# Optimization experiments

Hardware: AMD Instinct MI355X
Metric: run time of the kernel (lower is better)

Reference implementation:

```python
import jax, jax.numpy as jnp
import numpy as np

K = 3          # B-spline order (cubic)
G = 10         # number of spline intervals over [0, 1]
NELY, NELX = 512, 512
WIDTHS = [2, 32, 32, 1]


def _make_grid(in_dim):
    # extended uniform knot vector over [0,1] with K extra knots each side: (in_dim, G+2K+1)
    h = 1.0 / G
    knots = jnp.arange(-K, G + K + 1, dtype=jnp.float32) * h
    return jnp.tile(knots[None, :], (in_dim, 1))


def setup_inputs() -> dict:
    key = jax.random.key(0)
    ks = jax.random.split(key, 1 + 3 * (len(WIDTHS) - 1))
    inp = {"coords": jax.random.uniform(ks[0], (NELY * NELX, 2), dtype=jnp.float32)}
    for l, (i, o) in enumerate(zip(WIDTHS[:-1], WIDTHS[1:])):
        inp[f"grid{l}"] = _make_grid(i)
        inp[f"coef{l}"] = 0.1 * jax.random.normal(ks[1 + 3 * l], (i, o, G + K), dtype=jnp.float32)
        inp[f"sb{l}"] = jax.random.normal(ks[2 + 3 * l], (i, o), dtype=jnp.float32) / np.sqrt(i).astype(np.float32)
        inp[f"sp{l}"] = jnp.ones((i, o), dtype=jnp.float32)
    inp["density_bias"] = jnp.full((1,), np.float32(np.log(0.5 / (1.0 - 0.5 + 1e-8))))
    return inp


def _b_batch(x, grid):
    # Cox-de Boor recursion. x: (B, in), grid: (in, G+2K+1) -> bases (B, in, G+K)
    xe = x[:, :, None]
    v = ((xe >= grid[None, :, :-1]) & (xe < grid[None, :, 1:])).astype(x.dtype)
    for p in range(1, K + 1):
        left = (xe - grid[None, :, : -(p + 1)]) / (grid[None, :, p:-1] - grid[None, :, : -(p + 1)])
        right = (grid[None, :, p + 1:] - xe) / (grid[None, :, p + 1:] - grid[None, :, 1:-p])
        v = left * v[:, :, :-1] + right * v[:, :, 1:]
    return v


def _kan_layer(x, grid, coef, sb, sp):
    # y_out = sum_in [ sb * silu(x) + sp * sum_k B_k(x) * coef_k ]
    B = _b_batch(x, grid)                               # (batch, in, G+K)
    spline = jnp.einsum('bik,iok->bio', B, coef)        # (batch, in, out)
    base = jax.nn.silu(x)                               # (batch, in)
    return jnp.sum(sb[None] * base[:, :, None] + sp[None] * spline, axis=1)


def reference(coords, grid0, coef0, sb0, sp0, grid1, coef1, sb1, sp1,
              grid2, coef2, sb2, sp2, density_bias):
    h = _kan_layer(coords, grid0, coef0, sb0, sp0)
    h = _kan_layer(h, grid1, coef1, sb1, sp1)
    logits = _kan_layer(h, grid2, coef2, sb2, sp2) + density_bias
    return jax.nn.sigmoid(logits).reshape(1, NELY, NELX)
```

## Files before the change

kernel.cpp:

```cpp
#include <hip/hip_runtime.h>
#include <hip/hip_bf16.h>

typedef __hip_bfloat16 bf16;
typedef __fp16 h2v __attribute__((ext_vector_type(2)));
typedef __fp16 half8 __attribute__((ext_vector_type(8)));
typedef float floatx4 __attribute__((ext_vector_type(4)));

#define NPTS (512*512)

#define OFF_BIAS 12
#define OFF_FLAG 13
#define OFF_BF   16
#define NFRAG    50
#define WS_WORDS (16 + NFRAG*64*4)


__device__ __forceinline__ bool sniff_f32(const void* g0) {
    float f = ((const float*)g0)[0];
    return fabsf(f + 0.3f) < 0.01f;
}
__device__ __forceinline__ float ld(const void* p, int i, bool f32) {
    return f32 ? ((const float*)p)[i] : __bfloat162float(((const bf16*)p)[i]);
}
__device__ __forceinline__ unsigned pk_rtn(float a, float b) {
    union { h2v v; unsigned u; } x;
    x.v[0] = (__fp16)a; x.v[1] = (__fp16)b;
    return x.u;
}
__device__ __forceinline__ unsigned pkf16(float a, float b) {
    union { h2v v; unsigned u; } x;
    x.v = __builtin_amdgcn_cvt_pkrtz(a, b);
    return x.u;
}

__device__ float slotval(int layer, int K, int o,
                         const void* c0, const void* sb0, const void* sp0,
                         const void* c1, const void* sb1, const void* sp1,
                         const void* c2, const void* sb2, const void* sp2, bool f32)
{
    int i = K >> 4, s = K & 15;
    if (layer == 2 && o != 0) return 0.0f;
    if (s >= 1 && s <= 13) {
        int m = s - 1;
        if (layer == 0) return ld(c0, (i*32+o)*13 + m, f32) * ld(sp0, i*32+o, f32);
        if (layer == 1) return ld(c1, (i*32+o)*13 + m, f32) * ld(sp1, i*32+o, f32);
        return ld(c2, i*13 + m, f32) * ld(sp2, i, f32);
    }
    if (s == 14) {
        if (layer == 0) return ld(sb0, i*32+o, f32);
        if (layer == 1) return ld(sb1, i*32+o, f32);
        return ld(sb2, i, f32);
    }
    return 0.0f;
}

__global__ __launch_bounds__(256) void kan_prep(
    const void* __restrict__ g0, const void* __restrict__ c0,
    const void* __restrict__ sb0, const void* __restrict__ sp0,
    const void* __restrict__ g1, const void* __restrict__ c1,
    const void* __restrict__ sb1, const void* __restrict__ sp1,
    const void* __restrict__ g2, const void* __restrict__ c2,
    const void* __restrict__ sb2, const void* __restrict__ sp2,
    const void* __restrict__ bias, float* __restrict__ ws)
{
    const bool f32 = sniff_f32(g0);
    int t = blockIdx.x * blockDim.x + threadIdx.x;

    if (t < 16) {
        if (t < 12) {
            int l = t >> 2, j = t & 3;
            const void* g = (l == 0) ? g0 : (l == 1) ? g1 : g2;
            float lo = ld(g, 0, f32), hi = ld(g, 16, f32);
            float ih = 16.0f / (hi - lo);
            float v = (j == 0) ? lo : (j == 1) ? hi
                    : (j == 2) ? ih : (-lo * ih);
            ws[t] = v;
        } else if (t == 12) ws[12] = ld(bias, 0, f32);
        else if (t == 13)   ws[13] = f32 ? 1.0f : 0.0f;
        else                ws[t] = 0.0f;
        return;
    }
    int ft = t - 16;
    if (ft >= NFRAG * 64) return;
    int f = ft >> 6, l = ft & 63, n = l & 15, q = l >> 4;
    int layer, c, nt;
    if (f < 2)       { layer = 0; c = 0;          nt = f; }
    else if (f < 34) { layer = 1; c = (f - 2) >> 1; nt = (f - 2) & 1; }
    else             { layer = 2; c = f - 34;     nt = 0; }
    int o = nt * 16 + n;
    unsigned wv[4];
#pragma unroll
    for (int jp = 0; jp < 4; jp++) {
        int K0 = c * 32 + q * 8 + jp * 2;
        float v0 = slotval(layer, K0,     o, c0,sb0,sp0, c1,sb1,sp1, c2,sb2,sp2, f32);
        float v1 = slotval(layer, K0 + 1, o, c0,sb0,sp0, c1,sb1,sp1, c2,sb2,sp2, f32);
        wv[jp] = pk_rtn(v0, v1);
    }
    uint4 out4; out4.x = wv[0]; out4.y = wv[1]; out4.z = wv[2]; out4.w = wv[3];
    ((uint4*)((unsigned*)ws + OFF_BF))[f * 64 + l] = out4;
}

__device__ __forceinline__ floatx4 mf(uint4 a, uint4 b, floatx4 c)
{
    union { uint4 u; half8 h; } ua, ub;
    ua.u = a; ub.u = b;
    return __builtin_amdgcn_mfma_f32_16x16x32_f16(ua.h, ub.h, c, 0, 0, 0);
}

__device__ __forceinline__ void eval_taps(float x, float ngh, float ih,
    unsigned& A, unsigned& B, unsigned& C, int& wout, float& si)
{
    float t  = fmaf(x, ih, ngh);
    float fj = floorf(t);
    float u  = t - fj;
    bool inb = (t >= 0.0f) && (t < 16.0f);
    float s6 = inb ? 0.166666667f : 0.0f;
    int jc = min(max((int)fj, 0), 15);
    float u2 = u * u, u3 = u2 * u, om = 1.0f - u;
    float b0 = om * om * om * s6;
    float b1 = (fmaf(3.0f, u3, 4.0f) - 6.0f * u2) * s6;
    float b2 = fmaf(-3.0f, u3, fmaf(3.0f, u2, fmaf(3.0f, u, 1.0f))) * s6;
    float b3 = u3 * s6;
    int s0 = jc - 2;
    wout = ((s0 + 2) >> 1) - 1;
    if (s0 & 1) { A = pkf16(0.0f, b0); B = pkf16(b1, b2); C = pkf16(b3, 0.0f); }
    else        { A = pkf16(b0, b1);   B = pkf16(b2, b3); C = 0u; }
    si = x / (1.0f + __expf(-x));
}

struct TapPack {
    unsigned A0, B0, C0, A1, B1, C1, S0, S1;
    int w0, w1;
};

__device__ __forceinline__ TapPack eval2(float f0, float f1,
                                         float ngh, float ih)
{
    TapPack t;
    float si0, si1;
    eval_taps(f0, ngh, ih, t.A0, t.B0, t.C0, t.w0, si0);
    eval_taps(f1, ngh, ih, t.A1, t.B1, t.C1, t.w1, si1);
    t.S0 = pkf16(si0, 0.0f);
    t.S1 = pkf16(si1, 0.0f);
    return t;
}

__device__ __forceinline__ void commit(unsigned* row, const TapPack& t)
{
    uint4 z; z.x = 0u; z.y = 0u; z.z = 0u; z.w = 0u;
    *(uint4*)(row + 0)  = z;
    *(uint4*)(row + 4)  = z;
    *(uint4*)(row + 8)  = z;
    *(uint4*)(row + 12) = z;
    row[t.w0 < 0 ? 18 : t.w0] = t.A0;
    row[t.w0 + 1]  = t.B0;
    row[t.w0 + 2]  = t.C0;
    row[8 + t.w1]  = t.A1;
    row[9 + t.w1]  = t.B1;
    row[10 + t.w1] = t.C1;
    row[7]  = t.S0;
    row[15] = t.S1;
}

__global__ __launch_bounds__(256, 4) void kan_main(
    const void* __restrict__ coords, const float* __restrict__ ws,
    void* __restrict__ out)
{
    __shared__ __align__(16) unsigned lds[4 * 1280];
    const unsigned* wsu = (const unsigned*)ws;
    const uint4* bfp = (const uint4*)(wsu + OFF_BF);

    int tid = threadIdx.x;
    int l = tid & 63, w = tid >> 6;
    int p = blockIdx.x * 256 + w * 64 + l;

    unsigned* rb = lds + w * 1280;
    unsigned* cb = rb;
    unsigned* myrow = cb + l * 20;

    const bool f32 = (ws[OFF_FLAG] != 0.0f);
    float x0, x1;
    if (f32) {
        float2 c = ((const float2*)coords)[p];
        x0 = c.x; x1 = c.y;
    } else {
        unsigned cc = ((const unsigned*)coords)[p];
        union { unsigned u; float f; } cv;
        cv.u = (cc & 0xffffu) << 16;  x0 = cv.f;
        cv.u = cc & 0xffff0000u;      x1 = cv.f;
    }

    const float iha = ws[2],  ngha = ws[3];
    const float ihb = ws[6],  nghb = ws[7];
    const float ihc = ws[10], nghc = ws[11];

    const int arow = l & 15, aq = (l >> 4) * 4;
    const int drow = (l >> 4) * 4, dcol = l & 15;

    float h[32];

    {
        floatx4 acc[4][2];
#pragma unroll
        for (int mt = 0; mt < 4; mt++)
#pragma unroll
            for (int nt = 0; nt < 2; nt++) acc[mt][nt] = (floatx4)0.0f;

        uint4 bf0 = bfp[0 * 64 + l], bf1 = bfp[1 * 64 + l];
        TapPack t0 = eval2(x0, x1, ngha, iha);
        commit(myrow, t0);
#pragma unroll
        for (int mt = 0; mt < 4; mt++) {
            uint4 a = *(const uint4*)(cb + (arow + 16 * mt) * 20 + aq);
            acc[mt][0] = mf(a, bf0, acc[mt][0]);
            acc[mt][1] = mf(a, bf1, acc[mt][1]);
        }
#pragma unroll
        for (int nt = 0; nt < 2; nt++) {
#pragma unroll
            for (int mt = 0; mt < 4; mt++)
#pragma unroll
                for (int r = 0; r < 4; r++)
                    rb[(mt*16 + drow + r) * 20 + dcol] =
                        __float_as_uint(acc[mt][nt][r]);
#pragma unroll
            for (int q = 0; q < 4; q++) {
                uint4 v = *(const uint4*)(rb + l * 20 + q * 4);
                h[nt*16 + q*4+0] = __uint_as_float(v.x);
                h[nt*16 + q*4+1] = __uint_as_float(v.y);
                h[nt*16 + q*4+2] = __uint_as_float(v.z);
                h[nt*16 + q*4+3] = __uint_as_float(v.w);
            }
        }
    }

    {
        floatx4 acc[4][2];
#pragma unroll
        for (int mt = 0; mt < 4; mt++)
#pragma unroll
            for (int nt = 0; nt < 2; nt++) acc[mt][nt] = (floatx4)0.0f;

        uint4 bf0 = bfp[2 * 64 + l], bf1 = bfp[3 * 64 + l];
        {
            TapPack t0 = eval2(h[0], h[1], nghb, ihb);
            commit(myrow, t0);
        }
#pragma unroll
        for (int c = 0; c < 16; c++) {
            uint4 nbf0, nbf1; TapPack tn;
            if (c < 15) {
                nbf0 = bfp[(4 + 2*c) * 64 + l];
                nbf1 = bfp[(5 + 2*c) * 64 + l];
                tn = eval2(h[2*c + 2], h[2*c + 3], nghb, ihb);
            }
#pragma unroll
            for (int mt = 0; mt < 4; mt++) {
                uint4 a = *(const uint4*)(cb + (arow + 16 * mt) * 20 + aq);
                acc[mt][0] = mf(a, bf0, acc[mt][0]);
                acc[mt][1] = mf(a, bf1, acc[mt][1]);
            }
            if (c < 15) { commit(myrow, tn); bf0 = nbf0; bf1 = nbf1; }
        }
#pragma unroll
        for (int nt = 0; nt < 2; nt++) {
#pragma unroll
            for (int mt = 0; mt < 4; mt++)
#pragma unroll
                for (int r = 0; r < 4; r++)
                    rb[(mt*16 + drow + r) * 20 + dcol] =
                        __float_as_uint(acc[mt][nt][r]);
#pragma unroll
            for (int q = 0; q < 4; q++) {
                uint4 v = *(const uint4*)(rb + l * 20 + q * 4);
                h[nt*16 + q*4+0] = __uint_as_float(v.x);
                h[nt*16 + q*4+1] = __uint_as_float(v.y);
                h[nt*16 + q*4+2] = __uint_as_float(v.z);
                h[nt*16 + q*4+3] = __uint_as_float(v.w);
            }
        }
    }

    {
        floatx4 acc[4];
#pragma unroll
        for (int mt = 0; mt < 4; mt++) acc[mt] = (floatx4)0.0f;

        uint4 bf = bfp[34 * 64 + l];
        {
            TapPack t0 = eval2(h[0], h[1], nghc, ihc);
            commit(myrow, t0);
        }
#pragma unroll
        for (int c = 0; c < 16; c++) {
            uint4 nbf; TapPack tn;
            if (c < 15) {
                nbf = bfp[(35 + c) * 64 + l];
                tn = eval2(h[2*c + 2], h[2*c + 3], nghc, ihc);
            }
#pragma unroll
            for (int mt = 0; mt < 4; mt++) {
                uint4 a = *(const uint4*)(cb + (arow + 16 * mt) * 20 + aq);
                acc[mt] = mf(a, bf, acc[mt]);
            }
            if (c < 15) { commit(myrow, tn); bf = nbf; }
        }
        if ((l & 15) == 0) {
#pragma unroll
            for (int mt = 0; mt < 4; mt++)
#pragma unroll
                for (int r = 0; r < 4; r++)
                    rb[(mt*16 + drow + r) * 20] = __float_as_uint(acc[mt][r]);
        }
        float z = __uint_as_float(rb[l * 20]);
        float r = 1.0f / (1.0f + __expf(-(z + ws[OFF_BIAS])));
        if (f32) ((float*)out)[p] = r;
        else     ((bf16*)out)[p] = __float2bfloat16(r);
    }
}

extern "C" void kernel_launch(void* const* d_in, const int* in_sizes, int n_in,
                              void* d_out, int out_size, void* d_ws, size_t ws_size,
                              hipStream_t stream)
{
    float* ws = (float*)d_ws;

    kan_prep<<<(16 + NFRAG*64 + 255) / 256, 256, 0, stream>>>(
        d_in[1], d_in[2], d_in[3], d_in[4],
        d_in[5], d_in[6], d_in[7], d_in[8],
        d_in[9], d_in[10], d_in[11], d_in[12],
        d_in[13], ws);

    kan_main<<<NPTS / 256, 256, 0, stream>>>(d_in[0], ws, d_out);
}
```

Measured before the change: 121.0 us.

## Replace final-layer MFMA with per-thread scalar spline lookup from LDS table

Result: faster. 112.2 us (-7.2%).

```diff
diff --git a/kernel.cpp b/kernel.cpp
--- a/kernel.cpp
+++ b/kernel.cpp
@@ -11,8 +11,9 @@
 #define OFF_BIAS 12
 #define OFF_FLAG 13
 #define OFF_BF   16
-#define NFRAG    50
-#define WS_WORDS (16 + NFRAG*64*4)
+#define NFRAG    34
+#define OFF_LIN  (16 + NFRAG*256)
+#define LIN_WORDS 640
 
 
 __device__ __forceinline__ bool sniff_f32(const void* g0) {
@@ -36,20 +37,17 @@
 __device__ float slotval(int layer, int K, int o,
                          const void* c0, const void* sb0, const void* sp0,
                          const void* c1, const void* sb1, const void* sp1,
-                         const void* c2, const void* sb2, const void* sp2, bool f32)
+                         bool f32)
 {
     int i = K >> 4, s = K & 15;
-    if (layer == 2 && o != 0) return 0.0f;
     if (s >= 1 && s <= 13) {
         int m = s - 1;
         if (layer == 0) return ld(c0, (i*32+o)*13 + m, f32) * ld(sp0, i*32+o, f32);
-        if (layer == 1) return ld(c1, (i*32+o)*13 + m, f32) * ld(sp1, i*32+o, f32);
-        return ld(c2, i*13 + m, f32) * ld(sp2, i, f32);
+        return ld(c1, (i*32+o)*13 + m, f32) * ld(sp1, i*32+o, f32);
     }
     if (s == 14) {
         if (layer == 0) return ld(sb0, i*32+o, f32);
-        if (layer == 1) return ld(sb1, i*32+o, f32);
-        return ld(sb2, i, f32);
+        return ld(sb1, i*32+o, f32);
     }
     return 0.0f;
 }
@@ -81,23 +79,32 @@
         return;
     }
     int ft = t - 16;
-    if (ft >= NFRAG * 64) return;
-    int f = ft >> 6, l = ft & 63, n = l & 15, q = l >> 4;
-    int layer, c, nt;
-    if (f < 2)       { layer = 0; c = 0;          nt = f; }
-    else if (f < 34) { layer = 1; c = (f - 2) >> 1; nt = (f - 2) & 1; }
-    else             { layer = 2; c = f - 34;     nt = 0; }
-    int o = nt * 16 + n;
-    unsigned wv[4];
-#pragma unroll
-    for (int jp = 0; jp < 4; jp++) {
-        int K0 = c * 32 + q * 8 + jp * 2;
-        float v0 = slotval(layer, K0,     o, c0,sb0,sp0, c1,sb1,sp1, c2,sb2,sp2, f32);
-        float v1 = slotval(layer, K0 + 1, o, c0,sb0,sp0, c1,sb1,sp1, c2,sb2,sp2, f32);
-        wv[jp] = pk_rtn(v0, v1);
-    }
-    uint4 out4; out4.x = wv[0]; out4.y = wv[1]; out4.z = wv[2]; out4.w = wv[3];
-    ((uint4*)((unsigned*)ws + OFF_BF))[f * 64 + l] = out4;
+    if (ft < NFRAG * 64) {
+        int f = ft >> 6, l = ft & 63, n = l & 15, q = l >> 4;
+        int layer, c, nt;
+        if (f < 2) { layer = 0; c = 0;            nt = f; }
+        else       { layer = 1; c = (f - 2) >> 1; nt = (f - 2) & 1; }
+        int o = nt * 16 + n;
+        unsigned wv[4];
+#pragma unroll
+        for (int jp = 0; jp < 4; jp++) {
+            int K0 = c * 32 + q * 8 + jp * 2;
+            float v0 = slotval(layer, K0,     o, c0,sb0,sp0, c1,sb1,sp1, f32);
+            float v1 = slotval(layer, K0 + 1, o, c0,sb0,sp0, c1,sb1,sp1, f32);
+            wv[jp] = pk_rtn(v0, v1);
+        }
+        uint4 out4; out4.x = wv[0]; out4.y = wv[1]; out4.z = wv[2]; out4.w = wv[3];
+        ((uint4*)((unsigned*)ws + OFF_BF))[f * 64 + l] = out4;
+        return;
+    }
+    int w2 = ft - NFRAG * 64;
+    if (w2 < LIN_WORDS) {
+        int i = w2 / 20, j = w2 - i * 20;
+        float v = 0.0f;
+        if (j >= 3 && j <= 15) v = ld(c2, i*13 + (j - 3), f32) * ld(sp2, i, f32);
+        else if (j == 19)      v = ld(sb2, i, f32);
+        ws[OFF_LIN + w2] = v;
+    }
 }
 
 __device__ __forceinline__ floatx4 mf(uint4 a, uint4 b, floatx4 c)
@@ -166,13 +173,21 @@
     const void* __restrict__ coords, const float* __restrict__ ws,
     void* __restrict__ out)
 {
-    __shared__ __align__(16) unsigned lds[4 * 1280];
+    __shared__ __align__(16) unsigned lds[4 * 1280 + LIN_WORDS];
     const unsigned* wsu = (const unsigned*)ws;
     const uint4* bfp = (const uint4*)(wsu + OFF_BF);
 
     int tid = threadIdx.x;
     int l = tid & 63, w = tid >> 6;
     int p = blockIdx.x * 256 + w * 64 + l;
+
+    unsigned* lin2s = lds + 4 * 1280;
+#pragma unroll
+    for (int j = 0; j < 3; j++) {
+        int idx = tid + j * 256;
+        if (idx < LIN_WORDS) lin2s[idx] = wsu[OFF_LIN + idx];
+    }
+    __syncthreads();
 
     unsigned* rb = lds + w * 1280;
     unsigned* cb = rb;
@@ -282,38 +297,32 @@
     }
 
     {
-        floatx4 acc[4];
-#pragma unroll
-        for (int mt = 0; mt < 4; mt++) acc[mt] = (floatx4)0.0f;
-
-        uint4 bf = bfp[34 * 64 + l];
-        {
-            TapPack t0 = eval2(h[0], h[1], nghc, ihc);
-            commit(myrow, t0);
-        }
-#pragma unroll
-        for (int c = 0; c < 16; c++) {
-            uint4 nbf; TapPack tn;
-            if (c < 15) {
-                nbf = bfp[(35 + c) * 64 + l];
-                tn = eval2(h[2*c + 2], h[2*c + 3], nghc, ihc);
-            }
-#pragma unroll
-            for (int mt = 0; mt < 4; mt++) {
-                uint4 a = *(const uint4*)(cb + (arow + 16 * mt) * 20 + aq);
-                acc[mt] = mf(a, bf, acc[mt]);
-            }
-            if (c < 15) { commit(myrow, tn); bf = nbf; }
-        }
-        if ((l & 15) == 0) {
-#pragma unroll
-            for (int mt = 0; mt < 4; mt++)
-#pragma unroll
-                for (int r = 0; r < 4; r++)
-                    rb[(mt*16 + drow + r) * 20] = __float_as_uint(acc[mt][r]);
-        }
-        float z = __uint_as_float(rb[l * 20]);
-        float r = 1.0f / (1.0f + __expf(-(z + ws[OFF_BIAS])));
+        const float* l2t = (const float*)lin2s;
+        float z0 = ws[OFF_BIAS], z1 = 0.0f, z2 = 0.0f, z3 = 0.0f;
+#pragma unroll
+        for (int i = 0; i < 32; i++) {
+            float x = h[i];
+            float t  = fmaf(x, ihc, nghc);
+            float fj = floorf(t);
+            float u  = t - fj;
+            bool inb = (t >= 0.0f) && (t < 16.0f);
+            float s6 = inb ? 0.166666667f : 0.0f;
+            int jc = min(max((int)fj, 0), 15);
+            float u2 = u * u, u3 = u2 * u, om = 1.0f - u;
+            float b0 = om * om * om * s6;
+            float b1 = (fmaf(3.0f, u3, 4.0f) - 6.0f * u2) * s6;
+            float b2 = fmaf(-3.0f, u3, fmaf(3.0f, u2, fmaf(3.0f, u, 1.0f))) * s6;
+            float b3 = u3 * s6;
+            const float* row = l2t + i * 20;
+            float si = x / (1.0f + __expf(-x));
+            z0 = fmaf(b0, row[jc + 0], z0);
+            z1 = fmaf(b1, row[jc + 1], z1);
+            z2 = fmaf(b2, row[jc + 2], z2);
+            z3 = fmaf(b3, row[jc + 3], z3);
+            z0 = fmaf(si, row[19], z0);
+        }
+        float z = (z0 + z1) + (z2 + z3);
+        float r = 1.0f / (1.0f + __expf(-z));
         if (f32) ((float*)out)[p] = r;
         else     ((bf16*)out)[p] = __float2bfloat16(r);
     }
@@ -325,7 +334,7 @@
 {
     float* ws = (float*)d_ws;
 
-    kan_prep<<<(16 + NFRAG*64 + 255) / 256, 256, 0, stream>>>(
+    kan_prep<<<(16 + NFRAG*64 + LIN_WORDS + 255) / 256, 256, 0, stream>>>(
         d_in[1], d_in[2], d_in[3], d_in[4],
         d_in[5], d_in[6], d_in[7], d_in[8],
         d_in[9], d_in[10], d_in[11], d_in[12],
```
